# Kernel optimization log

Hardware: AMD Instinct MI355X
Metric: run time of the kernel (lower is better)

Reference implementation:

```python
import jax, jax.numpy as jnp
import numpy as np

B, T, H = 128, 2048, 128

def setup_inputs() -> dict:
    key = jax.random.key(0)
    k1, k2, k3, k4, k5, k6 = jax.random.split(key, 6)
    s = 1.0 / np.sqrt(H)
    return {
        "H_pos": jax.random.normal(k1, (B, T, H), jnp.float32),
        "H_dyn": jax.random.normal(k2, (B, T, H), jnp.float32),
        "acc_w": jax.random.uniform(k3, (B, T), jnp.float32),
        "W_h": jax.random.uniform(k4, (H, H), jnp.float32, -s, s),
        "W_d": jax.random.uniform(k5, (H, H), jnp.float32, -s, s),
        "W_a": jax.random.uniform(k6, (H,), jnp.float32, -s, s),
        "b_a": jnp.zeros((), jnp.float32),
        "beta": jnp.zeros((), jnp.float32),
    }

def reference(H_pos, H_dyn, acc_w, W_h, W_d, W_a, b_a, beta):
    # energy: W_a(tanh(W_h H_pos + W_d H_dyn)) -> [B, T]
    z = jnp.tanh(jnp.einsum('bth,oh->bto', H_pos, W_h)
                 + jnp.einsum('bth,oh->bto', H_dyn, W_d))
    energy = jnp.einsum('bth,h->bt', z, W_a) + b_a
    # acceleration normalization
    acc_norm = acc_w / jnp.clip(jnp.max(acc_w, axis=1, keepdims=True), 1e-6)
    beta_pos = jax.nn.softplus(beta)
    alpha = jax.nn.softmax(energy * (1.0 + beta_pos * acc_norm), axis=1)  # [B, T]
    context = jnp.einsum('bt,bth->bh', alpha, H_pos)  # [B, H]
    return (context, alpha)
```

## Files before the change

### kernel.cpp

```cpp
#include <hip/hip_runtime.h>
#include <hip/hip_bf16.h>

#define B_ 128
#define T_ 2048
#define H_ 128

typedef __attribute__((ext_vector_type(8))) short short8;
typedef __attribute__((ext_vector_type(4))) float f32x4;

__device__ __forceinline__ short8 pack8(const float4 x, const float4 y) {
    union { __hip_bfloat162 h2[4]; short8 s; } u;
    u.h2[0] = __float22bfloat162_rn(make_float2(x.x, x.y));
    u.h2[1] = __float22bfloat162_rn(make_float2(x.z, x.w));
    u.h2[2] = __float22bfloat162_rn(make_float2(y.x, y.y));
    u.h2[3] = __float22bfloat162_rn(make_float2(y.z, y.w));
    return u.s;
}
__device__ __forceinline__ float tanh_fast(float x) {
    x = fminf(fmaxf(x, -20.f), 20.f);
    float e = __expf(2.f * x);
    return (e - 1.f) / (e + 1.f);
}

__global__ __launch_bounds__(512) void energy_kernel(
    const float* __restrict__ Hp,
    const float* __restrict__ Hd,
    const float* __restrict__ Wh,
    const float* __restrict__ Wd,
    const float* __restrict__ Wa,
    const float* __restrict__ ba_p,
    float* __restrict__ energy,
    int ntiles)
{
    __shared__ unsigned short Bfrag[64 * 64 * 8];
    __shared__ float Was[H_];

    const int tid = threadIdx.x;

    #pragma unroll
    for (int p = 0; p < 8; p++) {
        int fl = p * 512 + tid;
        int f  = fl >> 6;
        int l  = fl & 63;
        int kt = f >> 3, nt = f & 7;
        int o   = nt * 16 + (l & 15);
        int col = kt * 32 + ((l >> 4) << 3);
        const float* src = (kt < 4) ? (Wh + o * H_ + col) : (Wd + o * H_ + (col - 128));
        float4 x0 = *(const float4*)src;
        float4 x1 = *(const float4*)(src + 4);
        *(short8*)&Bfrag[fl * 8] = pack8(x0, x1);
    }
    if (tid < H_) Was[tid] = Wa[tid];
    __syncthreads();

    const float ba = ba_p[0];

    const int wave = tid >> 6;
    const int lane = tid & 63;
    const int l15  = lane & 15;
    const int lq   = lane >> 4;

    for (int tile = blockIdx.x; tile < ntiles; tile += gridDim.x) {
        const int row0 = tile * 256 + wave * 32;
        const float* a0p = Hp + (size_t)(row0 + l15) * H_ + lq * 8;
        const float* a1p = a0p + 16 * H_;
        const float* a0d = Hd + (size_t)(row0 + l15) * H_ + lq * 8;
        const float* a1d = a0d + 16 * H_;

        f32x4 acc0[8], acc1[8];
        #pragma unroll
        for (int nt = 0; nt < 8; nt++) {
            acc0[nt] = (f32x4){0.f, 0.f, 0.f, 0.f};
            acc1[nt] = (f32x4){0.f, 0.f, 0.f, 0.f};
        }

        float4 p00 = *(const float4*)(a0p), p01 = *(const float4*)(a0p + 4);
        float4 p10 = *(const float4*)(a1p), p11 = *(const float4*)(a1p + 4);

        #pragma unroll 1
        for (int kt = 0; kt < 8; kt++) {
            float4 n00 = p00, n01 = p01, n10 = p10, n11 = p11;
            if (kt < 7) {
                int ktn = kt + 1;
                const float* q0 = (ktn < 4) ? (a0p + ktn * 32) : (a0d + (ktn - 4) * 32);
                const float* q1 = (ktn < 4) ? (a1p + ktn * 32) : (a1d + (ktn - 4) * 32);
                n00 = *(const float4*)q0; n01 = *(const float4*)(q0 + 4);
                n10 = *(const float4*)q1; n11 = *(const float4*)(q1 + 4);
            }
            short8 af0 = pack8(p00, p01);
            short8 af1 = pack8(p10, p11);
            const unsigned short* bp = &Bfrag[kt * 8 * 512 + lane * 8];
            #pragma unroll
            for (int nt = 0; nt < 8; nt++) {
                short8 bf = *(const short8*)(bp + nt * 512);
                acc0[nt] = __builtin_amdgcn_mfma_f32_16x16x32_bf16(af0, bf, acc0[nt], 0, 0, 0);
                acc1[nt] = __builtin_amdgcn_mfma_f32_16x16x32_bf16(af1, bf, acc1[nt], 0, 0, 0);
            }
            p00 = n00; p01 = n01; p10 = n10; p11 = n11;
        }

        float ep0[4] = {0.f, 0.f, 0.f, 0.f};
        float ep1[4] = {0.f, 0.f, 0.f, 0.f};
        #pragma unroll
        for (int nt = 0; nt < 8; nt++) {
            const float wa = Was[nt * 16 + l15];
            #pragma unroll
            for (int r = 0; r < 4; r++) {
                ep0[r] += tanh_fast(acc0[nt][r]) * wa;
                ep1[r] += tanh_fast(acc1[nt][r]) * wa;
            }
        }
        #pragma unroll
        for (int m = 1; m < 16; m <<= 1) {
            #pragma unroll
            for (int r = 0; r < 4; r++) {
                ep0[r] += __shfl_xor(ep0[r], m, 64);
                ep1[r] += __shfl_xor(ep1[r], m, 64);
            }
        }
        if (l15 == 0) {
            #pragma unroll
            for (int r = 0; r < 4; r++) {
                energy[row0 + lq * 4 + r]      = ep0[r] + ba;
                energy[row0 + 16 + lq * 4 + r] = ep1[r] + ba;
            }
        }
    }
}

__global__ __launch_bounds__(256) void softmax_ctx_kernel(
    const float* __restrict__ Hp,
    const float* __restrict__ accw,
    const float* __restrict__ beta_p,
    const float* __restrict__ energy,
    float* __restrict__ out_alpha,
    float* __restrict__ cpart)
{
    __shared__ float al_s[T_];
    __shared__ float red[8 * H_];
    __shared__ float sred[8];

    const int sl   = blockIdx.x & 15;
    const int b    = blockIdx.x >> 4;
    const int tid  = threadIdx.x;
    const int lane = tid & 63;
    const int wid  = tid >> 6;

    const float beta_pos = log1pf(__expf(beta_p[0]));

    float av[8], ev[8];
    {
        const float* pa = accw + b * T_ + tid * 8;
        const float* pe = energy + b * T_ + tid * 8;
        float4 a0 = *(const float4*)pa, a1 = *(const float4*)(pa + 4);
        float4 e0 = *(const float4*)pe, e1 = *(const float4*)(pe + 4);
        av[0]=a0.x; av[1]=a0.y; av[2]=a0.z; av[3]=a0.w;
        av[4]=a1.x; av[5]=a1.y; av[6]=a1.z; av[7]=a1.w;
        ev[0]=e0.x; ev[1]=e0.y; ev[2]=e0.z; ev[3]=e0.w;
        ev[4]=e1.x; ev[5]=e1.y; ev[6]=e1.z; ev[7]=e1.w;
    }
    float amax = -1e30f;
    #pragma unroll
    for (int i = 0; i < 8; i++) amax = fmaxf(amax, av[i]);
    for (int m = 32; m >= 1; m >>= 1) amax = fmaxf(amax, __shfl_xor(amax, m, 64));
    if (lane == 0) sred[wid] = amax;
    __syncthreads();
    if (tid == 0)
        sred[4] = fmaxf(fmaxf(sred[0], sred[1]), fmaxf(sred[2], sred[3]));
    __syncthreads();
    const float invd = beta_pos / fmaxf(sred[4], 1e-6f);

    float sv[8], smax = -1e30f;
    #pragma unroll
    for (int i = 0; i < 8; i++) {
        sv[i] = ev[i] * (1.f + av[i] * invd);
        smax = fmaxf(smax, sv[i]);
    }
    for (int m = 32; m >= 1; m >>= 1) smax = fmaxf(smax, __shfl_xor(smax, m, 64));
    __syncthreads();
    if (lane == 0) sred[wid] = smax;
    __syncthreads();
    if (tid == 0)
        sred[5] = fmaxf(fmaxf(sred[0], sred[1]), fmaxf(sred[2], sred[3]));
    __syncthreads();
    const float smax_all = sred[5];

    float p[8], psum = 0.f;
    #pragma unroll
    for (int i = 0; i < 8; i++) { p[i] = __expf(sv[i] - smax_all); psum += p[i]; }
    for (int m = 32; m >= 1; m >>= 1) psum += __shfl_xor(psum, m, 64);
    __syncthreads();
    if (lane == 0) sred[wid] = psum;
    __syncthreads();
    if (tid == 0)
        sred[6] = sred[0] + sred[1] + sred[2] + sred[3];
    __syncthreads();
    const float invS = 1.f / sred[6];

    #pragma unroll
    for (int i = 0; i < 8; i++) al_s[tid * 8 + i] = p[i] * invS;
    __syncthreads();

    if (tid < 128)
        out_alpha[b * T_ + sl * 128 + tid] = al_s[sl * 128 + tid];

    const int row = tid >> 5;
    const int c4  = tid & 31;

    const float* base = Hp + ((size_t)b * T_ + sl * 128) * H_ + c4 * 4;
    const float* al   = al_s + sl * 128;

    float4 s0 = {0,0,0,0}, s1 = {0,0,0,0}, s2 = {0,0,0,0}, s3 = {0,0,0,0};
    #pragma unroll
    for (int it = 0; it < 16; it += 4) {
        int t0 = (it + 0) * 8 + row, t1 = (it + 1) * 8 + row;
        int t2 = (it + 2) * 8 + row, t3 = (it + 3) * 8 + row;
        float a0 = al[t0], a1 = al[t1], a2 = al[t2], a3 = al[t3];
        float4 v0 = *(const float4*)(base + (size_t)t0 * H_);
        float4 v1 = *(const float4*)(base + (size_t)t1 * H_);
        float4 v2 = *(const float4*)(base + (size_t)t2 * H_);
        float4 v3 = *(const float4*)(base + (size_t)t3 * H_);
        s0.x += a0*v0.x; s0.y += a0*v0.y; s0.z += a0*v0.z; s0.w += a0*v0.w;
        s1.x += a1*v1.x; s1.y += a1*v1.y; s1.z += a1*v1.z; s1.w += a1*v1.w;
        s2.x += a2*v2.x; s2.y += a2*v2.y; s2.z += a2*v2.z; s2.w += a2*v2.w;
        s3.x += a3*v3.x; s3.y += a3*v3.y; s3.z += a3*v3.z; s3.w += a3*v3.w;
    }
    s0.x += s1.x + s2.x + s3.x;
    s0.y += s1.y + s2.y + s3.y;
    s0.z += s1.z + s2.z + s3.z;
    s0.w += s1.w + s2.w + s3.w;

    red[row * H_ + c4 * 4 + 0] = s0.x;
    red[row * H_ + c4 * 4 + 1] = s0.y;
    red[row * H_ + c4 * 4 + 2] = s0.z;
    red[row * H_ + c4 * 4 + 3] = s0.w;
    __syncthreads();
    if (tid < H_) {
        float s = 0.f;
        #pragma unroll
        for (int g = 0; g < 8; g++) s += red[g * H_ + tid];
        cpart[(b * 16 + sl) * H_ + tid] = s;
    }
}

__global__ __launch_bounds__(256) void ctx_reduce_kernel(
    const float* __restrict__ cpart, float* __restrict__ out_ctx)
{
    int i = blockIdx.x * 256 + threadIdx.x;
    if (i < B_ * H_) {
        int b = i >> 7, h = i & 127;
        float s = 0.f;
        #pragma unroll
        for (int g = 0; g < 16; g++) s += cpart[(b * 16 + g) * H_ + h];
        out_ctx[i] = s;
    }
}

extern "C" void kernel_launch(void* const* d_in, const int* in_sizes, int n_in,
                              void* d_out, int out_size, void* d_ws, size_t ws_size,
                              hipStream_t stream) {
    const float* Hp   = (const float*)d_in[0];
    const float* Hd   = (const float*)d_in[1];
    const float* accw = (const float*)d_in[2];
    const float* Wh   = (const float*)d_in[3];
    const float* Wd   = (const float*)d_in[4];
    const float* Wa   = (const float*)d_in[5];
    const float* ba   = (const float*)d_in[6];
    const float* beta = (const float*)d_in[7];

    float* energy_ws = (float*)d_ws;
    float* cpart_ws  = energy_ws + B_ * T_;

    float* out_ctx   = (float*)d_out;
    float* out_alpha = out_ctx + B_ * H_;

    const int ntiles = (B_ * T_) / 256;
    energy_kernel<<<512, 512, 0, stream>>>(Hp, Hd, Wh, Wd, Wa, ba, energy_ws, ntiles);
    softmax_ctx_kernel<<<B_ * 16, 256, 0, stream>>>(Hp, accw, beta, energy_ws, out_alpha, cpart_ws);
    ctx_reduce_kernel<<<(B_ * H_ + 255) / 256, 256, 0, stream>>>(cpart_ws, out_ctx);
}
```

Before: 322.3 us.

## Load all A operands up front per 16-row tile and widen context-sum loads

The energy kernel now handles 16 rows per wave instead of 32. It issues all eight K-chunk loads of H_pos and H_dyn at once, before the MFMA loop, instead of software-prefetching one chunk per iteration. This raises memory-level parallelism per wave and drops the loop-carried prefetch, at the cost of more registers held at once and reusing each B fragment for half as many rows. The context-sum loop in the softmax kernel also batches eight independent float4 loads per group to increase outstanding memory requests.

```diff
diff --git a/kernel.cpp b/kernel.cpp
--- a/kernel.cpp
+++ b/kernel.cpp
@@ -61,69 +61,52 @@
     const int lq   = lane >> 4;
 
     for (int tile = blockIdx.x; tile < ntiles; tile += gridDim.x) {
-        const int row0 = tile * 256 + wave * 32;
-        const float* a0p = Hp + (size_t)(row0 + l15) * H_ + lq * 8;
-        const float* a1p = a0p + 16 * H_;
-        const float* a0d = Hd + (size_t)(row0 + l15) * H_ + lq * 8;
-        const float* a1d = a0d + 16 * H_;
-
-        f32x4 acc0[8], acc1[8];
-        #pragma unroll
-        for (int nt = 0; nt < 8; nt++) {
-            acc0[nt] = (f32x4){0.f, 0.f, 0.f, 0.f};
-            acc1[nt] = (f32x4){0.f, 0.f, 0.f, 0.f};
-        }
-
-        float4 p00 = *(const float4*)(a0p), p01 = *(const float4*)(a0p + 4);
-        float4 p10 = *(const float4*)(a1p), p11 = *(const float4*)(a1p + 4);
-
-        #pragma unroll 1
+        const int row0 = tile * 128 + wave * 16;
+        const float* ap = Hp + (size_t)(row0 + l15) * H_ + lq * 8;
+        const float* ad = Hd + (size_t)(row0 + l15) * H_ + lq * 8;
+
+        float4 raw[16];
+        #pragma unroll
+        for (int c = 0; c < 4; c++) {
+            raw[2 * c]         = *(const float4*)(ap + c * 32);
+            raw[2 * c + 1]     = *(const float4*)(ap + c * 32 + 4);
+            raw[8 + 2 * c]     = *(const float4*)(ad + c * 32);
+            raw[8 + 2 * c + 1] = *(const float4*)(ad + c * 32 + 4);
+        }
+        short8 af[8];
+        #pragma unroll
+        for (int c = 0; c < 8; c++) af[c] = pack8(raw[2 * c], raw[2 * c + 1]);
+
+        f32x4 acc[8];
+        #pragma unroll
+        for (int nt = 0; nt < 8; nt++) acc[nt] = (f32x4){0.f, 0.f, 0.f, 0.f};
+
+        #pragma unroll
         for (int kt = 0; kt < 8; kt++) {
-            float4 n00 = p00, n01 = p01, n10 = p10, n11 = p11;
-            if (kt < 7) {
-                int ktn = kt + 1;
-                const float* q0 = (ktn < 4) ? (a0p + ktn * 32) : (a0d + (ktn - 4) * 32);
-                const float* q1 = (ktn < 4) ? (a1p + ktn * 32) : (a1d + (ktn - 4) * 32);
-                n00 = *(const float4*)q0; n01 = *(const float4*)(q0 + 4);
-                n10 = *(const float4*)q1; n11 = *(const float4*)(q1 + 4);
-            }
-            short8 af0 = pack8(p00, p01);
-            short8 af1 = pack8(p10, p11);
-            const unsigned short* bp = &Bfrag[kt * 8 * 512 + lane * 8];
+            const unsigned short* bp = &Bfrag[kt * 4096 + lane * 8];
             #pragma unroll
             for (int nt = 0; nt < 8; nt++) {
                 short8 bf = *(const short8*)(bp + nt * 512);
-                acc0[nt] = __builtin_amdgcn_mfma_f32_16x16x32_bf16(af0, bf, acc0[nt], 0, 0, 0);
-                acc1[nt] = __builtin_amdgcn_mfma_f32_16x16x32_bf16(af1, bf, acc1[nt], 0, 0, 0);
+                acc[nt] = __builtin_amdgcn_mfma_f32_16x16x32_bf16(af[kt], bf, acc[nt], 0, 0, 0);
             }
-            p00 = n00; p01 = n01; p10 = n10; p11 = n11;
-        }
-
-        float ep0[4] = {0.f, 0.f, 0.f, 0.f};
-        float ep1[4] = {0.f, 0.f, 0.f, 0.f};
+        }
+
+        float ep[4] = {0.f, 0.f, 0.f, 0.f};
         #pragma unroll
         for (int nt = 0; nt < 8; nt++) {
             const float wa = Was[nt * 16 + l15];
             #pragma unroll
-            for (int r = 0; r < 4; r++) {
-                ep0[r] += tanh_fast(acc0[nt][r]) * wa;
-                ep1[r] += tanh_fast(acc1[nt][r]) * wa;
-            }
+            for (int r = 0; r < 4; r++) ep[r] += tanh_fast(acc[nt][r]) * wa;
         }
         #pragma unroll
         for (int m = 1; m < 16; m <<= 1) {
             #pragma unroll
-            for (int r = 0; r < 4; r++) {
-                ep0[r] += __shfl_xor(ep0[r], m, 64);
-                ep1[r] += __shfl_xor(ep1[r], m, 64);
-            }
+            for (int r = 0; r < 4; r++) ep[r] += __shfl_xor(ep[r], m, 64);
         }
         if (l15 == 0) {
             #pragma unroll
-            for (int r = 0; r < 4; r++) {
-                energy[row0 + lq * 4 + r]      = ep0[r] + ba;
-                energy[row0 + 16 + lq * 4 + r] = ep1[r] + ba;
-            }
+            for (int r = 0; r < 4; r++)
+                energy[row0 + lq * 4 + r] = ep[r] + ba;
         }
     }
 }
@@ -210,36 +193,41 @@
     const float* base = Hp + ((size_t)b * T_ + sl * 128) * H_ + c4 * 4;
     const float* al   = al_s + sl * 128;
 
-    float4 s0 = {0,0,0,0}, s1 = {0,0,0,0}, s2 = {0,0,0,0}, s3 = {0,0,0,0};
-    #pragma unroll
-    for (int it = 0; it < 16; it += 4) {
-        int t0 = (it + 0) * 8 + row, t1 = (it + 1) * 8 + row;
-        int t2 = (it + 2) * 8 + row, t3 = (it + 3) * 8 + row;
-        float a0 = al[t0], a1 = al[t1], a2 = al[t2], a3 = al[t3];
-        float4 v0 = *(const float4*)(base + (size_t)t0 * H_);
-        float4 v1 = *(const float4*)(base + (size_t)t1 * H_);
-        float4 v2 = *(const float4*)(base + (size_t)t2 * H_);
-        float4 v3 = *(const float4*)(base + (size_t)t3 * H_);
-        s0.x += a0*v0.x; s0.y += a0*v0.y; s0.z += a0*v0.z; s0.w += a0*v0.w;
-        s1.x += a1*v1.x; s1.y += a1*v1.y; s1.z += a1*v1.z; s1.w += a1*v1.w;
-        s2.x += a2*v2.x; s2.y += a2*v2.y; s2.z += a2*v2.z; s2.w += a2*v2.w;
-        s3.x += a3*v3.x; s3.y += a3*v3.y; s3.z += a3*v3.z; s3.w += a3*v3.w;
-    }
-    s0.x += s1.x + s2.x + s3.x;
-    s0.y += s1.y + s2.y + s3.y;
-    s0.z += s1.z + s2.z + s3.z;
-    s0.w += s1.w + s2.w + s3.w;
-
-    red[row * H_ + c4 * 4 + 0] = s0.x;
-    red[row * H_ + c4 * 4 + 1] = s0.y;
-    red[row * H_ + c4 * 4 + 2] = s0.z;
-    red[row * H_ + c4 * 4 + 3] = s0.w;
+    float4 s[8];
+    #pragma unroll
+    for (int j = 0; j < 8; j++) s[j] = (float4){0.f, 0.f, 0.f, 0.f};
+
+    #pragma unroll
+    for (int g = 0; g < 2; g++) {
+        float  a[8];
+        float4 v[8];
+        #pragma unroll
+        for (int j = 0; j < 8; j++) {
+            int t = (g * 8 + j) * 8 + row;
+            v[j] = *(const float4*)(base + (size_t)t * H_);
+            a[j] = al[t];
+        }
+        #pragma unroll
+        for (int j = 0; j < 8; j++) {
+            s[j].x += a[j] * v[j].x; s[j].y += a[j] * v[j].y;
+            s[j].z += a[j] * v[j].z; s[j].w += a[j] * v[j].w;
+        }
+    }
+    #pragma unroll
+    for (int j = 1; j < 8; j++) {
+        s[0].x += s[j].x; s[0].y += s[j].y; s[0].z += s[j].z; s[0].w += s[j].w;
+    }
+
+    red[row * H_ + c4 * 4 + 0] = s[0].x;
+    red[row * H_ + c4 * 4 + 1] = s[0].y;
+    red[row * H_ + c4 * 4 + 2] = s[0].z;
+    red[row * H_ + c4 * 4 + 3] = s[0].w;
     __syncthreads();
     if (tid < H_) {
-        float s = 0.f;
-        #pragma unroll
-        for (int g = 0; g < 8; g++) s += red[g * H_ + tid];
-        cpart[(b * 16 + sl) * H_ + tid] = s;
+        float ssum = 0.f;
+        #pragma unroll
+        for (int g = 0; g < 8; g++) ssum += red[g * H_ + tid];
+        cpart[(b * 16 + sl) * H_ + tid] = ssum;
     }
 }
 
@@ -274,7 +262,7 @@
     float* out_ctx   = (float*)d_out;
     float* out_alpha = out_ctx + B_ * H_;
 
-    const int ntiles = (B_ * T_) / 256;
+    const int ntiles = (B_ * T_) / 128;
     energy_kernel<<<512, 512, 0, stream>>>(Hp, Hd, Wh, Wd, Wa, ba, energy_ws, ntiles);
     softmax_ctx_kernel<<<B_ * 16, 256, 0, stream>>>(Hp, accw, beta, energy_ws, out_alpha, cpart_ws);
     ctx_reduce_kernel<<<(B_ * H_ + 255) / 256, 256, 0, stream>>>(cpart_ws, out_ctx);
```

New measurement: 397.1 us. +23.2%, slower.
